# Kernel tuning notes

Hardware: AMD Instinct MI355X
Metric: run time of the kernel (lower is better)

Reference implementation:

```python
import jax, jax.numpy as jnp
from jax import lax
import numpy as np

B, H, W_, C, F = 4, 32, 32, 16, 16
KH, KW = 3, 3
L = 1.0


def setup_inputs() -> dict:
    key = jax.random.key(0)
    k1, k2, k3, k4 = jax.random.split(key, 4)
    inputs = jax.random.normal(k1, (B, H, W_, C), dtype=jnp.float32)
    # lecun_normal-style scales (stddev = 1/sqrt(fan_in))
    m_scale = 1.0 / np.sqrt(H * W_ * 1)
    g_scale = 1.0 / np.sqrt(KH * KW * C)
    M = jax.random.normal(k2, (H, W_, 1, H, W_, 1), dtype=jnp.float32) * m_scale
    Wp = jax.random.normal(k3, (H, W_, 1, H, W_, 1), dtype=jnp.float32) * m_scale
    G = jax.random.normal(k4, (H, W_, KH, KW, C, F), dtype=jnp.float32) * g_scale
    return {"inputs": inputs, "M": M, "Wp": Wp, "G": G}


def reference(inputs, M, Wp, G):
    b, h, w, c = inputs.shape
    kh, kw, f = G.shape[2], G.shape[3], G.shape[5]
    M2 = M[:, :, 0, :, :, 0]   # (i,j,p,q)
    W2 = Wp[:, :, 0, :, :, 0]  # (i,j,p,q)
    # first_term[b,i,j,c] = sum_pq M[i,j,p,q] * inputs[b,p,q,c]
    first = jnp.einsum('ijpq,bpqc->bijc', M2, inputs)
    # One big conv: kernel (kh,kw,c, h*w*f) gives shifted for every output pixel (i,j)
    K = jnp.transpose(G, (2, 3, 4, 0, 1, 5)).reshape(kh, kw, c, h * w * f)
    shifted = lax.conv_general_dilated(
        inputs, K, window_strides=(1, 1), padding='SAME',
        dimension_numbers=('NHWC', 'HWIO', 'NHWC'))
    shifted = shifted.reshape(b, h, w, h, w, f)  # (b,p,q,i,j,f)
    diff = jax.nn.relu(inputs[:, :, :, None, None, :] - shifted)  # (b,p,q,i,j,c)
    # second_term[b,i,j,c] = sum_pq W[i,j,p,q] * relu(inputs - shifted)[b,p,q,i,j,c]
    second = jnp.einsum('ijpq,bpqijc->bijc', W2, diff)
    return first - L * second
```

## Files before the change

kernel.cpp:

```cpp
#include <hip/hip_runtime.h>


typedef __attribute__((ext_vector_type(8))) short bf16x8;
typedef __attribute__((ext_vector_type(4))) float f32x4;

__device__ inline unsigned short f2bf(float x) {
    unsigned u = __float_as_uint(x);
    u += 0x7FFFu + ((u >> 16) & 1u);
    return (unsigned short)(u >> 16);
}
__device__ inline unsigned pack2(float a, float b) {
    return (unsigned)f2bf(a) | ((unsigned)f2bf(b) << 16);
}

__global__ __launch_bounds__(256) void build_A(const float* __restrict__ inp,
                                               uint4* __restrict__ A) {
    const int row = blockIdx.x * 256 + threadIdx.x;
    const int b = row >> 10, pq = row & 1023;
    const int p = pq >> 5, q = pq & 31;
    const int tile = row >> 4, m = row & 15;
    const float* inb = inp + b * 16384;

#pragma unroll
    for (int tap = 0; tap < 9; ++tap) {
        const int dh = tap / 3, dw = tap % 3;
        const int pp = p + dh - 1, qq = q + dw - 1;
        const bool v = ((unsigned)pp < 32u) && ((unsigned)qq < 32u);
        uint4 lo = {0, 0, 0, 0}, hi = {0, 0, 0, 0};
        if (v) {
            const float4* s = (const float4*)(inb + (pp * 32 + qq) * 16);
            float4 f0 = s[0], f1 = s[1], f2 = s[2], f3 = s[3];
            lo.x = pack2(f0.x, f0.y); lo.y = pack2(f0.z, f0.w);
            lo.z = pack2(f1.x, f1.y); lo.w = pack2(f1.z, f1.w);
            hi.x = pack2(f2.x, f2.y); hi.y = pack2(f2.z, f2.w);
            hi.z = pack2(f3.x, f3.y); hi.w = pack2(f3.z, f3.w);
        }
        const int kk = tap >> 1, qa = (tap & 1) * 2;
        const int base = (tile * 5 + kk) * 64 + qa * 16 + m;
        A[base] = lo;
        A[base + 16] = hi;
    }
    const uint4 z = {0, 0, 0, 0};
    const int base = (tile * 5 + 4) * 64 + 2 * 16 + m;
    A[base] = z;
    A[base + 16] = z;
}

__global__ __launch_bounds__(512, 2) void inrf_main(
    const float* __restrict__ inp,
    const float* __restrict__ M,
    const float* __restrict__ Wp,
    const float* __restrict__ G,
    const uint4* __restrict__ Aw,
    float* __restrict__ out)
{
    const int bid = blockIdx.x;
    const int t = threadIdx.x;

    __shared__ __align__(16) float W2l[4096];
    __shared__ __align__(16) float M2l[4096];
    __shared__ __align__(16) float G_l[9216];
    __shared__ float red[8][64];

    {
        const float* Wg = Wp + bid * 4096;
        const float* Mg = M  + bid * 4096;
        for (int i = t; i < 4096; i += 512) { W2l[i] = Wg[i]; M2l[i] = Mg[i]; }
        const float* Gg = G + bid * 9216;
        for (int i = t; i < 9216; i += 512) G_l[i] = Gg[i];
    }
    __syncthreads();

    const int l = t & 63, w = t >> 6;
    const int quad = l >> 4, col = l & 15;
    const int b = w >> 1;

    bf16x8 Bf[4][5];
#pragma unroll
    for (int ij = 0; ij < 4; ++ij) {
#pragma unroll
        for (int kk = 0; kk < 5; ++kk) {
            bf16x8 f;
#pragma unroll
            for (int j = 0; j < 8; ++j) {
                const int k = kk * 32 + quad * 8 + j;
                const float v = (k < 144) ? G_l[ij * 2304 + k * 16 + col] : 0.f;
                f[j] = (short)f2bf(v);
            }
            Bf[ij][kk] = f;
        }
    }

    float accv[4] = {0.f, 0.f, 0.f, 0.f};
    const int tile0 = b * 64 + (w & 1) * 32;
    const float* inb = inp + b * 16384;

    uint4 Acur[5], Anxt[5];
    float vcur[4], vnxt[4];
    {
        const int tg = tile0;
#pragma unroll
        for (int kk = 0; kk < 5; ++kk) Acur[kk] = Aw[(tg * 5 + kk) * 64 + l];
        const int pqb = (tg & 63) * 16 + quad * 4;
#pragma unroll
        for (int r = 0; r < 4; ++r) vcur[r] = inb[(pqb + r) * 16 + col];
    }

    for (int i = 0; i < 32; ++i) {
        const int tg = tile0 + i;
        if (i < 31) {
            const int tn = tg + 1;
#pragma unroll
            for (int kk = 0; kk < 5; ++kk) Anxt[kk] = Aw[(tn * 5 + kk) * 64 + l];
            const int pqb = (tn & 63) * 16 + quad * 4;
#pragma unroll
            for (int r = 0; r < 4; ++r) vnxt[r] = inb[(pqb + r) * 16 + col];
        }

        f32x4 C[4];
#pragma unroll
        for (int ij = 0; ij < 4; ++ij) C[ij] = (f32x4){0.f, 0.f, 0.f, 0.f};
#pragma unroll
        for (int kk = 0; kk < 5; ++kk) {
            const bf16x8 a = __builtin_bit_cast(bf16x8, Acur[kk]);
#pragma unroll
            for (int ij = 0; ij < 4; ++ij)
                C[ij] = __builtin_amdgcn_mfma_f32_16x16x32_bf16(a, Bf[ij][kk], C[ij], 0, 0, 0);
        }

        const int pqb = (tg & 63) * 16 + quad * 4;
#pragma unroll
        for (int ij = 0; ij < 4; ++ij) {
            const float4 w2 = *(const float4*)&W2l[ij * 1024 + pqb];
            const float4 m2 = *(const float4*)&M2l[ij * 1024 + pqb];
            accv[ij] += m2.x * vcur[0] - w2.x * fmaxf(vcur[0] - C[ij][0], 0.f);
            accv[ij] += m2.y * vcur[1] - w2.y * fmaxf(vcur[1] - C[ij][1], 0.f);
            accv[ij] += m2.z * vcur[2] - w2.z * fmaxf(vcur[2] - C[ij][2], 0.f);
            accv[ij] += m2.w * vcur[3] - w2.w * fmaxf(vcur[3] - C[ij][3], 0.f);
        }

#pragma unroll
        for (int kk = 0; kk < 5; ++kk) Acur[kk] = Anxt[kk];
#pragma unroll
        for (int r = 0; r < 4; ++r) vcur[r] = vnxt[r];
    }

#pragma unroll
    for (int ij = 0; ij < 4; ++ij) {
        float v = accv[ij];
        v += __shfl_xor(v, 16);
        v += __shfl_xor(v, 32);
        if (l < 16) red[w][ij * 16 + l] = v;
    }
    __syncthreads();

    if (t < 256) {
        const int ob = t >> 6, oij = (t >> 4) & 3, oc = t & 15;
        const float r0 = red[ob * 2][oij * 16 + oc] + red[ob * 2 + 1][oij * 16 + oc];
        out[ob * 16384 + (bid * 4 + oij) * 16 + oc] = r0;
    }
}

extern "C" void kernel_launch(void* const* d_in, const int* in_sizes, int n_in,
                              void* d_out, int out_size, void* d_ws, size_t ws_size,
                              hipStream_t stream) {
    const float* inp = (const float*)d_in[0];
    const float* M   = (const float*)d_in[1];
    const float* Wp  = (const float*)d_in[2];
    const float* G   = (const float*)d_in[3];
    float* out = (float*)d_out;

    uint4* A = (uint4*)d_ws;
    build_A<<<dim3(16), dim3(256), 0, stream>>>(inp, A);
    inrf_main<<<dim3(256), dim3(512), 0, stream>>>(inp, M, Wp, G, A, out);
}
```

Measured before the change: 103.0 us.

## Move first-term einsum to prologue kernel and split main grid per batch

The first-term M·x contraction moves out of the main kernel into a widened prologue kernel. That kernel also builds the bf16 im2col buffer with one thread per (row, tap) across 416 blocks instead of 16. The main kernel now launches 1024 blocks of 256 threads, one per (pixel group, batch). It drops the M tile from LDS and subtracts the second term into the output the prologue already wrote. This gives more blocks and less LDS per block for better occupancy, but G and W are now loaded four times (once per batch) and the output is read back and modified.

```diff
diff --git a/kernel.cpp b/kernel.cpp
--- a/kernel.cpp
+++ b/kernel.cpp
@@ -13,22 +13,23 @@
     return (unsigned)f2bf(a) | ((unsigned)f2bf(b) << 16);
 }
 
-__global__ __launch_bounds__(256) void build_A(const float* __restrict__ inp,
-                                               uint4* __restrict__ A) {
-    const int row = blockIdx.x * 256 + threadIdx.x;
-    const int b = row >> 10, pq = row & 1023;
-    const int p = pq >> 5, q = pq & 31;
-    const int tile = row >> 4, m = row & 15;
-    const float* inb = inp + b * 16384;
-
-#pragma unroll
-    for (int tap = 0; tap < 9; ++tap) {
-        const int dh = tap / 3, dw = tap % 3;
+__global__ __launch_bounds__(256) void inrf_phase1(
+    const float* __restrict__ inp, const float* __restrict__ M,
+    uint4* __restrict__ A, float* __restrict__ out)
+{
+    const int bb = blockIdx.x, t = threadIdx.x;
+
+    if (bb < 144) {
+        const int gid = bb * 256 + t;
+        const int row = gid / 9, tap = gid - row * 9;
+        const int b = row >> 10, pq = row & 1023, p = pq >> 5, q = pq & 31;
+        const int tile = row >> 4, m = row & 15;
+        const int dh = tap / 3, dw = tap - dh * 3;
         const int pp = p + dh - 1, qq = q + dw - 1;
         const bool v = ((unsigned)pp < 32u) && ((unsigned)qq < 32u);
         uint4 lo = {0, 0, 0, 0}, hi = {0, 0, 0, 0};
         if (v) {
-            const float4* s = (const float4*)(inb + (pp * 32 + qq) * 16);
+            const float4* s = (const float4*)(inp + b * 16384 + (pp * 32 + qq) * 16);
             float4 f0 = s[0], f1 = s[1], f2 = s[2], f3 = s[3];
             lo.x = pack2(f0.x, f0.y); lo.y = pack2(f0.z, f0.w);
             lo.z = pack2(f1.x, f1.y); lo.w = pack2(f1.z, f1.w);
@@ -39,45 +40,77 @@
         const int base = (tile * 5 + kk) * 64 + qa * 16 + m;
         A[base] = lo;
         A[base + 16] = hi;
-    }
-    const uint4 z = {0, 0, 0, 0};
-    const int base = (tile * 5 + 4) * 64 + 2 * 16 + m;
-    A[base] = z;
-    A[base + 16] = z;
-}
-
-__global__ __launch_bounds__(512, 2) void inrf_main(
-    const float* __restrict__ inp,
-    const float* __restrict__ M,
-    const float* __restrict__ Wp,
-    const float* __restrict__ G,
-    const uint4* __restrict__ Aw,
+        return;
+    }
+    if (bb < 160) {
+        const int row = (bb - 144) * 256 + t;
+        const int tile = row >> 4, m = row & 15;
+        const uint4 z = {0, 0, 0, 0};
+        const int base = (tile * 5 + 4) * 64 + 32 + m;
+        A[base] = z;
+        A[base + 16] = z;
+        return;
+    }
+
+    __shared__ float M2l[4096];
+    __shared__ float4 red2[256];
+    const int g = bb - 160;
+    for (int i = t; i < 4096; i += 256) M2l[i] = M[g * 4096 + i];
+    __syncthreads();
+
+    const int chunk = t >> 6, rest = t & 63;
+    const int ijl = rest >> 4, b = (rest >> 2) & 3, cg = t & 3;
+    const float4* xb = (const float4*)(inp + b * 16384) + cg;
+    const float4* mrow = (const float4*)&M2l[ijl * 1024 + chunk * 256];
+    float4 s = {0.f, 0.f, 0.f, 0.f};
+    const int pq0 = chunk * 256;
+    for (int r = 0; r < 256; r += 4) {
+        const float4 mm = mrow[r >> 2];
+        const float4 x0 = xb[(pq0 + r + 0) * 4];
+        const float4 x1 = xb[(pq0 + r + 1) * 4];
+        const float4 x2 = xb[(pq0 + r + 2) * 4];
+        const float4 x3 = xb[(pq0 + r + 3) * 4];
+        s.x += mm.x * x0.x + mm.y * x1.x + mm.z * x2.x + mm.w * x3.x;
+        s.y += mm.x * x0.y + mm.y * x1.y + mm.z * x2.y + mm.w * x3.y;
+        s.z += mm.x * x0.z + mm.y * x1.z + mm.z * x2.z + mm.w * x3.z;
+        s.w += mm.x * x0.w + mm.y * x1.w + mm.z * x2.w + mm.w * x3.w;
+    }
+    red2[t] = s;
+    __syncthreads();
+    if (t < 64) {
+        const float4 a = red2[t], b4 = red2[t + 64], c4 = red2[t + 128], d4 = red2[t + 192];
+        float4 r;
+        r.x = (a.x + b4.x) + (c4.x + d4.x);
+        r.y = (a.y + b4.y) + (c4.y + d4.y);
+        r.z = (a.z + b4.z) + (c4.z + d4.z);
+        r.w = (a.w + b4.w) + (c4.w + d4.w);
+        const int oij = t >> 4, ob = (t >> 2) & 3, ocg = t & 3;
+        *(float4*)(out + ob * 16384 + (g * 4 + oij) * 16 + ocg * 4) = r;
+    }
+}
+
+__global__ __launch_bounds__(256, 2) void inrf_main(
+    const float* __restrict__ inp, const float* __restrict__ Wp,
+    const float* __restrict__ G, const uint4* __restrict__ Aw,
     float* __restrict__ out)
 {
     const int bid = blockIdx.x;
+    const int g = bid & 255, b = bid >> 8;
     const int t = threadIdx.x;
 
     __shared__ __align__(16) float W2l[4096];
-    __shared__ __align__(16) float M2l[4096];
     __shared__ __align__(16) float G_l[9216];
-    __shared__ float red[8][64];
-
-    {
-        const float* Wg = Wp + bid * 4096;
-        const float* Mg = M  + bid * 4096;
-        for (int i = t; i < 4096; i += 512) { W2l[i] = Wg[i]; M2l[i] = Mg[i]; }
-        const float* Gg = G + bid * 9216;
-        for (int i = t; i < 9216; i += 512) G_l[i] = Gg[i];
-    }
-    __syncthreads();
-
-    const int l = t & 63, w = t >> 6;
-    const int quad = l >> 4, col = l & 15;
-    const int b = w >> 1;
+    __shared__ float red[4][64];
+
+    for (int i = t; i < 4096; i += 256) W2l[i] = Wp[g * 4096 + i];
+    for (int i = t; i < 9216; i += 256) G_l[i] = G[g * 9216 + i];
+    __syncthreads();
+
+    const int w = t >> 6, l = t & 63, quad = l >> 4, col = l & 15;
 
     bf16x8 Bf[4][5];
 #pragma unroll
-    for (int ij = 0; ij < 4; ++ij) {
+    for (int ij = 0; ij < 4; ++ij)
 #pragma unroll
         for (int kk = 0; kk < 5; ++kk) {
             bf16x8 f;
@@ -89,26 +122,24 @@
             }
             Bf[ij][kk] = f;
         }
-    }
-
+
+    const float* inb = inp + b * 16384;
+    const int tile0 = b * 64 + w * 16;
     float accv[4] = {0.f, 0.f, 0.f, 0.f};
-    const int tile0 = b * 64 + (w & 1) * 32;
-    const float* inb = inp + b * 16384;
 
     uint4 Acur[5], Anxt[5];
     float vcur[4], vnxt[4];
     {
-        const int tg = tile0;
-#pragma unroll
-        for (int kk = 0; kk < 5; ++kk) Acur[kk] = Aw[(tg * 5 + kk) * 64 + l];
-        const int pqb = (tg & 63) * 16 + quad * 4;
+#pragma unroll
+        for (int kk = 0; kk < 5; ++kk) Acur[kk] = Aw[(tile0 * 5 + kk) * 64 + l];
+        const int pqb = (tile0 & 63) * 16 + quad * 4;
 #pragma unroll
         for (int r = 0; r < 4; ++r) vcur[r] = inb[(pqb + r) * 16 + col];
     }
 
-    for (int i = 0; i < 32; ++i) {
+    for (int i = 0; i < 16; ++i) {
         const int tg = tile0 + i;
-        if (i < 31) {
+        if (i < 15) {
             const int tn = tg + 1;
 #pragma unroll
             for (int kk = 0; kk < 5; ++kk) Anxt[kk] = Aw[(tn * 5 + kk) * 64 + l];
@@ -132,11 +163,10 @@
 #pragma unroll
         for (int ij = 0; ij < 4; ++ij) {
             const float4 w2 = *(const float4*)&W2l[ij * 1024 + pqb];
-            const float4 m2 = *(const float4*)&M2l[ij * 1024 + pqb];
-            accv[ij] += m2.x * vcur[0] - w2.x * fmaxf(vcur[0] - C[ij][0], 0.f);
-            accv[ij] += m2.y * vcur[1] - w2.y * fmaxf(vcur[1] - C[ij][1], 0.f);
-            accv[ij] += m2.z * vcur[2] - w2.z * fmaxf(vcur[2] - C[ij][2], 0.f);
-            accv[ij] += m2.w * vcur[3] - w2.w * fmaxf(vcur[3] - C[ij][3], 0.f);
+            accv[ij] += w2.x * fmaxf(vcur[0] - C[ij][0], 0.f)
+                      + w2.y * fmaxf(vcur[1] - C[ij][1], 0.f)
+                      + w2.z * fmaxf(vcur[2] - C[ij][2], 0.f)
+                      + w2.w * fmaxf(vcur[3] - C[ij][3], 0.f);
         }
 
 #pragma unroll
@@ -154,10 +184,10 @@
     }
     __syncthreads();
 
-    if (t < 256) {
-        const int ob = t >> 6, oij = (t >> 4) & 3, oc = t & 15;
-        const float r0 = red[ob * 2][oij * 16 + oc] + red[ob * 2 + 1][oij * 16 + oc];
-        out[ob * 16384 + (bid * 4 + oij) * 16 + oc] = r0;
+    if (t < 64) {
+        const int oij = t >> 4, oc = t & 15;
+        const float sec = red[0][t] + red[1][t] + red[2][t] + red[3][t];
+        out[b * 16384 + (g * 4 + oij) * 16 + oc] -= sec;
     }
 }
 
@@ -171,6 +201,6 @@
     float* out = (float*)d_out;
 
     uint4* A = (uint4*)d_ws;
-    build_A<<<dim3(16), dim3(256), 0, stream>>>(inp, A);
-    inrf_main<<<dim3(256), dim3(512), 0, stream>>>(inp, M, Wp, G, A, out);
-}
+    inrf_phase1<<<dim3(416), dim3(256), 0, stream>>>(inp, M, A, out);
+    inrf_main<<<dim3(1024), dim3(256), 0, stream>>>(inp, Wp, G, A, out);
+}
```

Result: slower. 115.4 us (+12.0%).

## Fuse im2col build into main kernel using padded swizzled LDS input tile

Applied to the files above, without the earlier changes.

Removes the separate build_A kernel and its global im2col workspace. Each block now stages a zero-padded bf16 copy of one batch image in LDS with a swizzle and gathers the MFMA A fragments from it directly. The grid is split per (output group, batch) into 1024 blocks of 256 threads, with G pre-transposed to bf16 in LDS. M and Wp are read straight from global memory instead of being staged. This saves a launch and the workspace round-trip, but every block re-reads G and re-packs the whole input image, so redundant per-block setup grows.

```diff
diff --git a/kernel.cpp b/kernel.cpp
--- a/kernel.cpp
+++ b/kernel.cpp
@@ -13,109 +13,106 @@
     return (unsigned)f2bf(a) | ((unsigned)f2bf(b) << 16);
 }
 
-__global__ __launch_bounds__(256) void build_A(const float* __restrict__ inp,
-                                               uint4* __restrict__ A) {
-    const int row = blockIdx.x * 256 + threadIdx.x;
-    const int b = row >> 10, pq = row & 1023;
-    const int p = pq >> 5, q = pq & 31;
-    const int tile = row >> 4, m = row & 15;
-    const float* inb = inp + b * 16384;
+__global__ __launch_bounds__(256, 2) void inrf_fused(
+    const float* __restrict__ inp,
+    const float* __restrict__ M,
+    const float* __restrict__ Wp,
+    const float* __restrict__ G,
+    float* __restrict__ out)
+{
+    const int bid = blockIdx.x;
+    const int g = bid >> 2, b = bid & 3;
+    const int t = threadIdx.x, w = t >> 6, l = t & 63;
+    const int quad = l >> 4, m = l & 15;
+    const int half = quad & 1;
 
-#pragma unroll
-    for (int tap = 0; tap < 9; ++tap) {
-        const int dh = tap / 3, dw = tap % 3;
-        const int pp = p + dh - 1, qq = q + dw - 1;
-        const bool v = ((unsigned)pp < 32u) && ((unsigned)qq < 32u);
-        uint4 lo = {0, 0, 0, 0}, hi = {0, 0, 0, 0};
-        if (v) {
-            const float4* s = (const float4*)(inb + (pp * 32 + qq) * 16);
-            float4 f0 = s[0], f1 = s[1], f2 = s[2], f3 = s[3];
+    __shared__ __align__(16) uint4 Xl[1156 * 2];
+    __shared__ __align__(16) short Gt[4 * 16 * 168];
+    __shared__ float red[4][64];
+
+    for (int i = t; i < 2312; i += 256) Xl[i] = (uint4){0, 0, 0, 0};
+    for (int i = t; i < 1536; i += 256) {
+        const int ij = i / 384, r2 = i - ij * 384;
+        const int cf = r2 / 24, kp = r2 - cf * 24;
+        Gt[(ij * 16 + cf) * 168 + 144 + kp] = 0;
+    }
+    for (int i = t; i < 9216; i += 256) {
+        const int ij = i / 2304, r2 = i - ij * 2304;
+        const int k = r2 >> 4, cf = r2 & 15;
+        Gt[(ij * 16 + cf) * 168 + k] = (short)f2bf(G[g * 9216 + i]);
+    }
+    __syncthreads();
+
+    {
+        const float4* xb = (const float4*)(inp + b * 16384);
+        for (int r = t; r < 1024; r += 256) {
+            const int p = r >> 5, q = r & 31;
+            const int hc = (p + 1) * 34 + (q + 1);
+            const float4 f0 = xb[r * 4 + 0], f1 = xb[r * 4 + 1];
+            const float4 f2 = xb[r * 4 + 2], f3 = xb[r * 4 + 3];
+            uint4 lo, hi;
             lo.x = pack2(f0.x, f0.y); lo.y = pack2(f0.z, f0.w);
             lo.z = pack2(f1.x, f1.y); lo.w = pack2(f1.z, f1.w);
             hi.x = pack2(f2.x, f2.y); hi.y = pack2(f2.z, f2.w);
             hi.z = pack2(f3.x, f3.y); hi.w = pack2(f3.z, f3.w);
+            const int sw = hc & 1;
+            Xl[2 * hc + sw] = lo;
+            Xl[2 * hc + (sw ^ 1)] = hi;
         }
-        const int kk = tap >> 1, qa = (tap & 1) * 2;
-        const int base = (tile * 5 + kk) * 64 + qa * 16 + m;
-        A[base] = lo;
-        A[base + 16] = hi;
     }
-    const uint4 z = {0, 0, 0, 0};
-    const int base = (tile * 5 + 4) * 64 + 2 * 16 + m;
-    A[base] = z;
-    A[base + 16] = z;
-}
 
-__global__ __launch_bounds__(512, 2) void inrf_main(
-    const float* __restrict__ inp,
-    const float* __restrict__ M,
-    const float* __restrict__ Wp,
-    const float* __restrict__ G,
-    const uint4* __restrict__ Aw,
-    float* __restrict__ out)
-{
-    const int bid = blockIdx.x;
-    const int t = threadIdx.x;
+    bf16x8 Bf[4][5];
+#pragma unroll
+    for (int ij = 0; ij < 4; ++ij)
+#pragma unroll
+        for (int kk = 0; kk < 5; ++kk)
+            Bf[ij][kk] = *(const bf16x8*)&Gt[(ij * 16 + m) * 168 + kk * 32 + quad * 8];
 
-    __shared__ __align__(16) float W2l[4096];
-    __shared__ __align__(16) float M2l[4096];
-    __shared__ __align__(16) float G_l[9216];
-    __shared__ float red[8][64];
-
-    {
-        const float* Wg = Wp + bid * 4096;
-        const float* Mg = M  + bid * 4096;
-        for (int i = t; i < 4096; i += 512) { W2l[i] = Wg[i]; M2l[i] = Mg[i]; }
-        const float* Gg = G + bid * 9216;
-        for (int i = t; i < 9216; i += 512) G_l[i] = Gg[i];
+    int K_[5];
+#pragma unroll
+    for (int kk = 0; kk < 5; ++kk) {
+        const int tap = 2 * kk + (quad >> 1);
+        const int dh = tap / 3, dw = tap - dh * 3;
+        K_[kk] = (dh * 34 + dw) * 32 + ((half ^ (dw & 1)) << 4);
     }
     __syncthreads();
 
-    const int l = t & 63, w = t >> 6;
-    const int quad = l >> 4, col = l & 15;
-    const int b = w >> 1;
+    const int tile0w = w * 16;
+    const float* wrow = Wp + g * 4096;
+    const float* mrow = M + g * 4096;
+    const float* xrow = inp + b * 16384 + m;
 
-    bf16x8 Bf[4][5];
-#pragma unroll
-    for (int ij = 0; ij < 4; ++ij) {
+    auto loadA = [&](int i, uint4* dst) {
+        const int pq = (tile0w + i) * 16 + m;
+        const int p = pq >> 5, q = pq & 31;
+        const int base = (p * 34 + q) * 32;
+        const int qo = (q & 1) << 4;
 #pragma unroll
         for (int kk = 0; kk < 5; ++kk) {
-            bf16x8 f;
-#pragma unroll
-            for (int j = 0; j < 8; ++j) {
-                const int k = kk * 32 + quad * 8 + j;
-                const float v = (k < 144) ? G_l[ij * 2304 + k * 16 + col] : 0.f;
-                f[j] = (short)f2bf(v);
-            }
-            Bf[ij][kk] = f;
+            int a = (base + K_[kk]) ^ qo;
+            if (kk == 4) a = (quad >= 2) ? 0 : a;
+            dst[kk] = *(const uint4*)((const char*)Xl + a);
         }
-    }
+    };
 
     float accv[4] = {0.f, 0.f, 0.f, 0.f};
-    const int tile0 = b * 64 + (w & 1) * 32;
-    const float* inb = inp + b * 16384;
+    uint4 Acur[5], Anxt[5];
+    loadA(0, Acur);
 
-    uint4 Acur[5], Anxt[5];
-    float vcur[4], vnxt[4];
-    {
-        const int tg = tile0;
+    for (int i = 0; i < 16; ++i) {
+        const int pqb = (tile0w + i) * 16 + quad * 4;
+
+        float4 w2[4], m2[4];
+        float xv[4];
 #pragma unroll
-        for (int kk = 0; kk < 5; ++kk) Acur[kk] = Aw[(tg * 5 + kk) * 64 + l];
-        const int pqb = (tg & 63) * 16 + quad * 4;
+        for (int ij = 0; ij < 4; ++ij) {
+            w2[ij] = *(const float4*)&wrow[ij * 1024 + pqb];
+            m2[ij] = *(const float4*)&mrow[ij * 1024 + pqb];
+        }
 #pragma unroll
-        for (int r = 0; r < 4; ++r) vcur[r] = inb[(pqb + r) * 16 + col];
-    }
+        for (int r = 0; r < 4; ++r) xv[r] = xrow[(pqb + r) * 16];
 
-    for (int i = 0; i < 32; ++i) {
-        const int tg = tile0 + i;
-        if (i < 31) {
-            const int tn = tg + 1;
-#pragma unroll
-            for (int kk = 0; kk < 5; ++kk) Anxt[kk] = Aw[(tn * 5 + kk) * 64 + l];
-            const int pqb = (tn & 63) * 16 + quad * 4;
-#pragma unroll
-            for (int r = 0; r < 4; ++r) vnxt[r] = inb[(pqb + r) * 16 + col];
-        }
+        if (i < 15) loadA(i + 1, Anxt);
 
         f32x4 C[4];
 #pragma unroll
@@ -128,21 +125,16 @@
                 C[ij] = __builtin_amdgcn_mfma_f32_16x16x32_bf16(a, Bf[ij][kk], C[ij], 0, 0, 0);
         }
 
-        const int pqb = (tg & 63) * 16 + quad * 4;
 #pragma unroll
         for (int ij = 0; ij < 4; ++ij) {
-            const float4 w2 = *(const float4*)&W2l[ij * 1024 + pqb];
-            const float4 m2 = *(const float4*)&M2l[ij * 1024 + pqb];
-            accv[ij] += m2.x * vcur[0] - w2.x * fmaxf(vcur[0] - C[ij][0], 0.f);
-            accv[ij] += m2.y * vcur[1] - w2.y * fmaxf(vcur[1] - C[ij][1], 0.f);
-            accv[ij] += m2.z * vcur[2] - w2.z * fmaxf(vcur[2] - C[ij][2], 0.f);
-            accv[ij] += m2.w * vcur[3] - w2.w * fmaxf(vcur[3] - C[ij][3], 0.f);
+            accv[ij] += m2[ij].x * xv[0] - w2[ij].x * fmaxf(xv[0] - C[ij][0], 0.f);
+            accv[ij] += m2[ij].y * xv[1] - w2[ij].y * fmaxf(xv[1] - C[ij][1], 0.f);
+            accv[ij] += m2[ij].z * xv[2] - w2[ij].z * fmaxf(xv[2] - C[ij][2], 0.f);
+            accv[ij] += m2[ij].w * xv[3] - w2[ij].w * fmaxf(xv[3] - C[ij][3], 0.f);
         }
 
 #pragma unroll
         for (int kk = 0; kk < 5; ++kk) Acur[kk] = Anxt[kk];
-#pragma unroll
-        for (int r = 0; r < 4; ++r) vcur[r] = vnxt[r];
     }
 
 #pragma unroll
@@ -154,10 +146,10 @@
     }
     __syncthreads();
 
-    if (t < 256) {
-        const int ob = t >> 6, oij = (t >> 4) & 3, oc = t & 15;
-        const float r0 = red[ob * 2][oij * 16 + oc] + red[ob * 2 + 1][oij * 16 + oc];
-        out[ob * 16384 + (bid * 4 + oij) * 16 + oc] = r0;
+    if (t < 64) {
+        const int oij = t >> 4, oc = t & 15;
+        const float r0 = red[0][t] + red[1][t] + red[2][t] + red[3][t];
+        out[b * 16384 + (g * 4 + oij) * 16 + oc] = r0;
     }
 }
 
@@ -170,7 +162,5 @@
     const float* G   = (const float*)d_in[3];
     float* out = (float*)d_out;
 
-    uint4* A = (uint4*)d_ws;
-    build_A<<<dim3(16), dim3(256), 0, stream>>>(inp, A);
-    inrf_main<<<dim3(256), dim3(512), 0, stream>>>(inp, M, Wp, G, A, out);
+    inrf_fused<<<dim3(1024), dim3(256), 0, stream>>>(inp, M, Wp, G, out);
 }
```

After: 105.3 us. +2.2%, slower.
